# Kernel optimization log

Measured on AMD Instinct MI355X. Metric: run time of the kernel, lower is better.

Reference implementation:

```python
import jax, jax.numpy as jnp
import numpy as np

N, E, D, H, G = 100000, 1250000, 64, 64, 128
GRAPH_ATTR_DIM = 4
BN_EPS = 1e-5


def setup_inputs() -> dict:
    key = jax.random.key(0)
    ks = jax.random.split(key, 32)
    inp = {
        "x": jax.random.normal(ks[0], (N, D), dtype=jnp.float32),
        "edge_index": jax.random.randint(ks[1], (2, E), 0, N, dtype=jnp.int64),
        "batch": jnp.sort(jax.random.randint(ks[2], (N,), 0, G, dtype=jnp.int64)),
        "graph_attr": jax.random.normal(ks[3], (G, GRAPH_ATTR_DIM), dtype=jnp.float32),
    }
    # SAGEConv params per layer: lin_l (neighbor path, with bias), lin_r (self path, no bias)
    dims = [(D, H), (H, H), (H, H)]
    kidx = 4
    for i, (din, dout) in enumerate(dims):
        s = 1.0 / np.sqrt(din)
        inp[f"Wl{i}"] = jax.random.uniform(ks[kidx + 0], (din, dout), minval=-s, maxval=s, dtype=jnp.float32)
        inp[f"bl{i}"] = jax.random.uniform(ks[kidx + 1], (dout,), minval=-s, maxval=s, dtype=jnp.float32)
        inp[f"Wr{i}"] = jax.random.uniform(ks[kidx + 2], (din, dout), minval=-s, maxval=s, dtype=jnp.float32)
        # BatchNorm1d (eval mode: running stats)
        inp[f"g{i}"] = jnp.ones((dout,), jnp.float32)
        inp[f"be{i}"] = jnp.zeros((dout,), jnp.float32)
        inp[f"rm{i}"] = jax.random.normal(ks[kidx + 3], (dout,), dtype=jnp.float32) * 0.1
        inp[f"rv{i}"] = jax.random.uniform(ks[kidx + 4], (dout,), minval=0.5, maxval=1.5, dtype=jnp.float32)
        kidx += 5
    clf_in, clf_h = H + GRAPH_ATTR_DIM, H // 2
    s1 = 1.0 / np.sqrt(clf_in)
    s2 = 1.0 / np.sqrt(clf_h)
    inp["W1"] = jax.random.uniform(ks[kidx + 0], (clf_in, clf_h), minval=-s1, maxval=s1, dtype=jnp.float32)
    inp["b1"] = jax.random.uniform(ks[kidx + 1], (clf_h,), minval=-s1, maxval=s1, dtype=jnp.float32)
    inp["W2"] = jax.random.uniform(ks[kidx + 2], (clf_h, 2), minval=-s2, maxval=s2, dtype=jnp.float32)
    inp["b2"] = jax.random.uniform(ks[kidx + 3], (2,), minval=-s2, maxval=s2, dtype=jnp.float32)
    return inp


def _sage_conv(x, src, dst, Wl, bl, Wr):
    # mean-aggregate neighbor messages x[src] onto dst nodes
    msg = x[src]                                            # [E, d]
    agg = jax.ops.segment_sum(msg, dst, num_segments=N)     # [N, d]
    cnt = jax.ops.segment_sum(jnp.ones((src.shape[0],), x.dtype), dst, num_segments=N)
    agg = agg / jnp.maximum(cnt, 1.0)[:, None]
    return agg @ Wl + bl + x @ Wr


def _bn_eval(x, g, be, rm, rv):
    return (x - rm) * (g * jax.lax.rsqrt(rv + BN_EPS)) + be


def reference(x, edge_index, batch, graph_attr,
              Wl0, bl0, Wr0, g0, be0, rm0, rv0,
              Wl1, bl1, Wr1, g1, be1, rm1, rv1,
              Wl2, bl2, Wr2, g2, be2, rm2, rv2,
              W1, b1, W2, b2):
    src, dst = edge_index[0], edge_index[1]
    layer_params = [
        (Wl0, bl0, Wr0, g0, be0, rm0, rv0),
        (Wl1, bl1, Wr1, g1, be1, rm1, rv1),
        (Wl2, bl2, Wr2, g2, be2, rm2, rv2),
    ]
    h = x
    for (Wl, bl, Wr, g, be, rm, rv) in layer_params:
        h = jax.nn.relu(_bn_eval(_sage_conv(h, src, dst, Wl, bl, Wr), g, be, rm, rv))
        # dropout is identity in eval mode
    # global mean pool over graphs
    gsum = jax.ops.segment_sum(h, batch, num_segments=G)
    gcnt = jax.ops.segment_sum(jnp.ones((h.shape[0],), h.dtype), batch, num_segments=G)
    gemb = gsum / jnp.maximum(gcnt, 1.0)[:, None]
    gemb = jnp.concatenate([gemb, graph_attr], axis=1)      # [G, H+4]
    return jax.nn.relu(gemb @ W1 + b1) @ W2 + b2             # [G, 2]
```

## Files before the change

### kernel.cpp

```cpp
#include <hip/hip_runtime.h>
#include <hip/hip_fp16.h>

#define DIM 64
#define NGRAPH 128
#define GATTR 4
#define BN_EPS 1e-5f
#define SCAN_CHUNK 4096
#define NPASS 4
#define XS 17


__global__ __launch_bounds__(256) void k_zero(int* __restrict__ cnt, int n,
                                              float* __restrict__ gsum,
                                              int* __restrict__ gcnt) {
    int stride = gridDim.x * 256;
    for (int i = blockIdx.x * 256 + threadIdx.x; i < n; i += stride) cnt[i] = 0;
    int i0 = blockIdx.x * 256 + threadIdx.x;
    if (i0 < NGRAPH * DIM) gsum[i0] = 0.f;
    if (i0 < NGRAPH) gcnt[i0] = 0;
}


__global__ __launch_bounds__(256) void k_cast(const float4* __restrict__ x4,
                                              uint2* __restrict__ o, int n4) {
    int stride = gridDim.x * 256;
    for (int i = blockIdx.x * 256 + threadIdx.x; i < n4; i += stride) {
        float4 v = x4[i];
        __half2 a = __float22half2_rn(make_float2(v.x, v.y));
        __half2 b = __float22half2_rn(make_float2(v.z, v.w));
        uint2 u;
        u.x = *(unsigned int*)&a;
        u.y = *(unsigned int*)&b;
        o[i] = u;
    }
}


__global__ __launch_bounds__(256) void k_count(const int* __restrict__ dst,
                                               int* __restrict__ cnt, int E) {
    int e = blockIdx.x * blockDim.x + threadIdx.x;
    if (e < E) atomicAdd(&cnt[dst[e]], 1);
}

__global__ __launch_bounds__(256) void k_scan1(const int* __restrict__ cnt,
                                               int* __restrict__ rowptr,
                                               int* __restrict__ partials, int n) {
    __shared__ int ws[256];
    int tid = threadIdx.x;
    int base = blockIdx.x * SCAN_CHUNK + tid * 16;
    int v[16];
    int s = 0;
#pragma unroll
    for (int i = 0; i < 16; ++i) {
        int idx = base + i;
        v[i] = (idx < n) ? cnt[idx] : 0;
        s += v[i];
    }
    ws[tid] = s;
    __syncthreads();
    for (int off = 1; off < 256; off <<= 1) {
        int t = (tid >= off) ? ws[tid - off] : 0;
        __syncthreads();
        ws[tid] += t;
        __syncthreads();
    }
    int excl = (tid == 0) ? 0 : ws[tid - 1];
    if (tid == 255) partials[blockIdx.x] = ws[255];
#pragma unroll
    for (int i = 0; i < 16; ++i) {
        int idx = base + i;
        if (idx < n) rowptr[idx] = excl;
        excl += v[i];
    }
}

__global__ __launch_bounds__(256) void k_scan23(int* __restrict__ rowptr,
                                                int* __restrict__ wp,
                                                const int* __restrict__ partials,
                                                int n, int E) {
    __shared__ int soff;
    if (threadIdx.x == 0) {
        int s = 0;
        for (int j = 0; j < blockIdx.x; ++j) s += partials[j];
        soff = s;
    }
    __syncthreads();
    int off = soff;
    int base = blockIdx.x * SCAN_CHUNK;
    for (int i = threadIdx.x; i < SCAN_CHUNK; i += 256) {
        int idx = base + i;
        if (idx < n) {
            int v = rowptr[idx] + off;
            rowptr[idx] = v;
            wp[idx] = v;
        }
    }
    if (blockIdx.x == 0 && threadIdx.x == 0) rowptr[n] = E;
}

__global__ __launch_bounds__(256) void k_scatter_pass(const int* __restrict__ src,
                                                      const int* __restrict__ dst,
                                                      int* __restrict__ wp,
                                                      int* __restrict__ col,
                                                      int E, int lo, int hi) {
    int e = blockIdx.x * blockDim.x + threadIdx.x;
    if (e >= E) return;
    int d = dst[e];
    if (d < lo || d >= hi) return;
    int p = atomicAdd(&wp[d], 1);
    col[p] = src[e];
}


__global__ __launch_bounds__(256) void k_agg(const __half* __restrict__ h16,
                                             const int* __restrict__ row_ptr,
                                             const int* __restrict__ col,
                                             float* __restrict__ agg, int n) {
    int wid = (blockIdx.x * blockDim.x + threadIdx.x) >> 6;
    if (wid >= n) return;
    int lane = threadIdx.x & 63;
    int g = lane >> 3;
    int p = lane & 7;
    int beg = row_ptr[wid], end = row_ptr[wid + 1];

    float a0 = 0.f, a1 = 0.f, a2 = 0.f, a3 = 0.f;
    float a4 = 0.f, a5 = 0.f, a6 = 0.f, a7 = 0.f;

#define ACCUM(V)                                                          \
    {                                                                     \
        const __half2* q = (const __half2*)&(V);                          \
        float2 f0 = __half22float2(q[0]);                                 \
        float2 f1 = __half22float2(q[1]);                                 \
        float2 f2 = __half22float2(q[2]);                                 \
        float2 f3 = __half22float2(q[3]);                                 \
        a0 += f0.x; a1 += f0.y; a2 += f1.x; a3 += f1.y;                   \
        a4 += f2.x; a5 += f2.y; a6 += f3.x; a7 += f3.y;                   \
    }

    int j = beg + g;
    for (; j + 8 < end; j += 16) {
        int s0 = col[j];
        int s1 = col[j + 8];
        uint4 v0 = ((const uint4*)(h16 + (size_t)s0 * DIM))[p];
        uint4 v1 = ((const uint4*)(h16 + (size_t)s1 * DIM))[p];
        ACCUM(v0)
        ACCUM(v1)
    }
    if (j < end) {
        int s0 = col[j];
        uint4 v0 = ((const uint4*)(h16 + (size_t)s0 * DIM))[p];
        ACCUM(v0)
    }
#undef ACCUM

#pragma unroll
    for (int m = 8; m <= 32; m <<= 1) {
        a0 += __shfl_xor(a0, m, 64);
        a1 += __shfl_xor(a1, m, 64);
        a2 += __shfl_xor(a2, m, 64);
        a3 += __shfl_xor(a3, m, 64);
        a4 += __shfl_xor(a4, m, 64);
        a5 += __shfl_xor(a5, m, 64);
        a6 += __shfl_xor(a6, m, 64);
        a7 += __shfl_xor(a7, m, 64);
    }

    if (g == 0) {
        float c = (float)(end - beg);
        float inv = 1.0f / fmaxf(c, 1.0f);
        float4* op = (float4*)(agg + (size_t)wid * DIM + p * 8);
        float4 r0, r1;
        r0.x = a0 * inv; r0.y = a1 * inv; r0.z = a2 * inv; r0.w = a3 * inv;
        r1.x = a4 * inv; r1.y = a5 * inv; r1.z = a6 * inv; r1.w = a7 * inv;
        op[0] = r0;
        op[1] = r1;
    }
}


__global__ __launch_bounds__(256) void k_xform(const float* __restrict__ agg,
                                               const __half* __restrict__ h16,
                                               const float* __restrict__ Wl,
                                               const float* __restrict__ bl,
                                               const float* __restrict__ Wr,
                                               const float* __restrict__ bng,
                                               const float* __restrict__ bnb,
                                               const float* __restrict__ bnm,
                                               const float* __restrict__ bnv,
                                               __half* __restrict__ out16, int n) {
    __shared__ float4 sWl[64 * 16];
    __shared__ float4 sWr[64 * 16];
    __shared__ float4 sA[64 * XS];
    __shared__ float4 sH[64 * XS];
    int tid = threadIdx.x;
    int base = blockIdx.x * 64;
    int rows = min(64, n - base);

    const float4* Wl4 = (const float4*)Wl;
    const float4* Wr4 = (const float4*)Wr;
    const float4* A4 = (const float4*)(agg + (size_t)base * DIM);
    const uint2* H2 = (const uint2*)(h16 + (size_t)base * DIM);
    for (int i = tid; i < 1024; i += 256) {
        sWl[i] = Wl4[i];
        sWr[i] = Wr4[i];
        int row = i >> 4, c = i & 15;
        float4 va = {0.f, 0.f, 0.f, 0.f}, vh = {0.f, 0.f, 0.f, 0.f};
        if (row < rows) {
            va = A4[i];
            uint2 u = H2[i];
            const __half2* q = (const __half2*)&u;
            float2 lo = __half22float2(q[0]);
            float2 hi = __half22float2(q[1]);
            vh.x = lo.x; vh.y = lo.y; vh.z = hi.x; vh.w = hi.y;
        }
        sA[row * XS + c] = va;
        sH[row * XS + c] = vh;
    }
    __syncthreads();

    int dq = tid & 15;
    int nq = tid >> 4;
    float4 acc0 = {0.f, 0.f, 0.f, 0.f};
    float4 acc1 = {0.f, 0.f, 0.f, 0.f};
    float4 acc2 = {0.f, 0.f, 0.f, 0.f};
    float4 acc3 = {0.f, 0.f, 0.f, 0.f};

    int arow = nq * 4 * XS;
#pragma unroll 4
    for (int kg = 0; kg < 16; ++kg) {
        float4 wl0 = sWl[(kg * 4 + 0) * 16 + dq];
        float4 wl1 = sWl[(kg * 4 + 1) * 16 + dq];
        float4 wl2 = sWl[(kg * 4 + 2) * 16 + dq];
        float4 wl3 = sWl[(kg * 4 + 3) * 16 + dq];
        float4 wr0 = sWr[(kg * 4 + 0) * 16 + dq];
        float4 wr1 = sWr[(kg * 4 + 1) * 16 + dq];
        float4 wr2 = sWr[(kg * 4 + 2) * 16 + dq];
        float4 wr3 = sWr[(kg * 4 + 3) * 16 + dq];
        float4 a0 = sA[arow + 0 * XS + kg];
        float4 a1 = sA[arow + 1 * XS + kg];
        float4 a2 = sA[arow + 2 * XS + kg];
        float4 a3 = sA[arow + 3 * XS + kg];
        float4 h0 = sH[arow + 0 * XS + kg];
        float4 h1 = sH[arow + 1 * XS + kg];
        float4 h2 = sH[arow + 2 * XS + kg];
        float4 h3 = sH[arow + 3 * XS + kg];
#define ACC1(AC, AV, HV)                                                        \
        AC.x += AV.x * wl0.x + AV.y * wl1.x + AV.z * wl2.x + AV.w * wl3.x       \
              + HV.x * wr0.x + HV.y * wr1.x + HV.z * wr2.x + HV.w * wr3.x;      \
        AC.y += AV.x * wl0.y + AV.y * wl1.y + AV.z * wl2.y + AV.w * wl3.y       \
              + HV.x * wr0.y + HV.y * wr1.y + HV.z * wr2.y + HV.w * wr3.y;      \
        AC.z += AV.x * wl0.z + AV.y * wl1.z + AV.z * wl2.z + AV.w * wl3.z       \
              + HV.x * wr0.z + HV.y * wr1.z + HV.z * wr2.z + HV.w * wr3.z;      \
        AC.w += AV.x * wl0.w + AV.y * wl1.w + AV.z * wl2.w + AV.w * wl3.w       \
              + HV.x * wr0.w + HV.y * wr1.w + HV.z * wr2.w + HV.w * wr3.w;
        ACC1(acc0, a0, h0)
        ACC1(acc1, a1, h1)
        ACC1(acc2, a2, h2)
        ACC1(acc3, a3, h3)
#undef ACC1
    }

    float4 g4 = ((const float4*)bng)[dq];
    float4 v4 = ((const float4*)bnv)[dq];
    float4 be4 = ((const float4*)bnb)[dq];
    float4 rm4 = ((const float4*)bnm)[dq];
    float4 bi4 = ((const float4*)bl)[dq];
    float4 sc;
    sc.x = g4.x / sqrtf(v4.x + BN_EPS);
    sc.y = g4.y / sqrtf(v4.y + BN_EPS);
    sc.z = g4.z / sqrtf(v4.z + BN_EPS);
    sc.w = g4.w / sqrtf(v4.w + BN_EPS);

    float4* accp[4] = {&acc0, &acc1, &acc2, &acc3};
#pragma unroll
    for (int i = 0; i < 4; ++i) {
        int node = base + nq * 4 + i;
        if (node < n) {
            float4 a = *accp[i];
            float4 r;
            r.x = fmaxf((a.x + bi4.x - rm4.x) * sc.x + be4.x, 0.f);
            r.y = fmaxf((a.y + bi4.y - rm4.y) * sc.y + be4.y, 0.f);
            r.z = fmaxf((a.z + bi4.z - rm4.z) * sc.z + be4.z, 0.f);
            r.w = fmaxf((a.w + bi4.w - rm4.w) * sc.w + be4.w, 0.f);
            __half2 o01 = __float22half2_rn(make_float2(r.x, r.y));
            __half2 o23 = __float22half2_rn(make_float2(r.z, r.w));
            uint2 u;
            u.x = *(unsigned int*)&o01;
            u.y = *(unsigned int*)&o23;
            ((uint2*)(out16 + (size_t)node * DIM))[dq] = u;
        }
    }
}


__global__ __launch_bounds__(256) void k_pool(const __half* __restrict__ h16,
                                              const int* __restrict__ batch,
                                              float* __restrict__ gsum,
                                              int* __restrict__ gcnt, int n) {
    int nw = gridDim.x * 4;
    int w = blockIdx.x * 4 + (threadIdx.x >> 6);
    int lane = threadIdx.x & 63;
    int chunk = (n + nw - 1) / nw;
    int s = w * chunk, e = min(s + chunk, n);
    if (s >= e) return;
    int cur = batch[s];
    float acc = 0.f;
    int cnt = 0;
    for (int i = s; i < e; ++i) {
        int g = batch[i];
        if (g != cur) {
            atomicAdd(&gsum[cur * DIM + lane], acc);
            if (lane == 0) atomicAdd(&gcnt[cur], cnt);
            acc = 0.f; cnt = 0; cur = g;
        }
        acc += __half2float(h16[(size_t)i * DIM + lane]);
        ++cnt;
    }
    atomicAdd(&gsum[cur * DIM + lane], acc);
    if (lane == 0) atomicAdd(&gcnt[cur], cnt);
}


__global__ __launch_bounds__(256) void k_mlp(const float* __restrict__ gsum,
                                             const int* __restrict__ gcnt,
                                             const float* __restrict__ gattr,
                                             const float* __restrict__ W1,
                                             const float* __restrict__ b1,
                                             const float* __restrict__ W2,
                                             const float* __restrict__ b2,
                                             float* __restrict__ out) {
    __shared__ float emb[NGRAPH][DIM + GATTR];
    __shared__ float hid[NGRAPH][32];
    int tid = threadIdx.x;
    for (int i = tid; i < NGRAPH * DIM; i += 256) {
        int g = i >> 6, d = i & 63;
        float c = (float)gcnt[g];
        emb[g][d] = gsum[i] / fmaxf(c, 1.0f);
    }
    for (int i = tid; i < NGRAPH * GATTR; i += 256) {
        int g = i >> 2, d = i & 3;
        emb[g][DIM + d] = gattr[i];
    }
    __syncthreads();
    for (int t = tid; t < NGRAPH * 32; t += 256) {
        int g = t >> 5, j = t & 31;
        float a = b1[j];
        for (int k = 0; k < DIM + GATTR; ++k) a += emb[g][k] * W1[k * 32 + j];
        hid[g][j] = fmaxf(a, 0.f);
    }
    __syncthreads();
    {
        int g = tid >> 1, o = tid & 1;
        float a = b2[o];
        for (int k = 0; k < 32; ++k) a += hid[g][k] * W2[k * 2 + o];
        out[g * 2 + o] = a;
    }
}

extern "C" void kernel_launch(void* const* d_in, const int* in_sizes, int n_in,
                              void* d_out, int out_size, void* d_ws, size_t ws_size,
                              hipStream_t stream) {
    const float* x = (const float*)d_in[0];
    const int* ei = (const int*)d_in[1];
    const int* batch = (const int*)d_in[2];
    const float* gattr = (const float*)d_in[3];
    const int N = in_sizes[0] / DIM;
    const int E = in_sizes[1] / 2;
    const int* src = ei;
    const int* dst = ei + E;

    const float *Wl[3], *bl[3], *Wr[3], *bg[3], *bb[3], *bm[3], *bv[3];
    for (int l = 0; l < 3; ++l) {
        int base = 4 + l * 7;
        Wl[l] = (const float*)d_in[base + 0];
        bl[l] = (const float*)d_in[base + 1];
        Wr[l] = (const float*)d_in[base + 2];
        bg[l] = (const float*)d_in[base + 3];
        bb[l] = (const float*)d_in[base + 4];
        bm[l] = (const float*)d_in[base + 5];
        bv[l] = (const float*)d_in[base + 6];
    }
    const float* W1 = (const float*)d_in[25];
    const float* b1 = (const float*)d_in[26];
    const float* W2 = (const float*)d_in[27];
    const float* b2 = (const float*)d_in[28];

    char* ws = (char*)d_ws;
    size_t off = 0;
    auto alloc = [&](size_t bytes) -> char* {
        char* p = ws + off;
        off += (bytes + 255) & ~(size_t)255;
        return p;
    };
    int* cnt = (int*)alloc((size_t)N * 4);
    int* rowptr = (int*)alloc((size_t)(N + 1) * 4);
    int* wp = (int*)alloc((size_t)N * 4);
    int* col = (int*)alloc((size_t)E * 4);
    float* aggb = (float*)alloc((size_t)N * DIM * 4);
    __half* x16 = (__half*)alloc((size_t)N * DIM * 2);
    __half* h16a = (__half*)alloc((size_t)N * DIM * 2);
    __half* h16b = (__half*)alloc((size_t)N * DIM * 2);
    float* gsum = (float*)alloc((size_t)NGRAPH * DIM * 4);
    int* gcnt = (int*)alloc((size_t)NGRAPH * 4);
    int* partials = (int*)alloc(1024 * 4);
    (void)ws_size;

    const int tpb = 256;
    const int nscan = (N + SCAN_CHUNK - 1) / SCAN_CHUNK;
    const int nbE = (E + tpb - 1) / tpb;

    k_zero<<<512, tpb, 0, stream>>>(cnt, N, gsum, gcnt);
    k_cast<<<1024, tpb, 0, stream>>>((const float4*)x, (uint2*)x16, N * DIM / 4);
    k_count<<<nbE, tpb, 0, stream>>>(dst, cnt, E);
    k_scan1<<<nscan, tpb, 0, stream>>>(cnt, rowptr, partials, N);
    k_scan23<<<nscan, tpb, 0, stream>>>(rowptr, wp, partials, N, E);
    {
        int per = (N + NPASS - 1) / NPASS;
        for (int p = 0; p < NPASS; ++p) {
            int lo = p * per;
            int hi = min(lo + per, N);
            if (lo >= hi) break;
            k_scatter_pass<<<nbE, tpb, 0, stream>>>(src, dst, wp, col, E, lo, hi);
        }
    }

    const __half* hin = x16;
    __half* houts[3] = {h16a, h16b, h16a};
    for (int l = 0; l < 3; ++l) {
        k_agg<<<(N * 64 + tpb - 1) / tpb, tpb, 0, stream>>>(hin, rowptr, col, aggb, N);
        k_xform<<<(N + 63) / 64, 256, 0, stream>>>(aggb, hin, Wl[l], bl[l], Wr[l],
                                                   bg[l], bb[l], bm[l], bv[l], houts[l], N);
        hin = houts[l];
    }

    k_pool<<<256, tpb, 0, stream>>>(hin, batch, gsum, gcnt, N);
    k_mlp<<<1, tpb, 0, stream>>>(gsum, gcnt, gattr, W1, b1, W2, b2, (float*)d_out);
}
```

Baseline: 537.6 us.

## Replace atomic CSR build with two-level bucketed counting sort

Builds the CSR adjacency with a bucket-level radix sort instead of global per-node atomic counting plus four scatter passes. Each block histograms its edge chunk into 128-node buckets in shared memory, a global scan yields offsets, edges are binned as (src,dst) pairs staged through shared memory, and a per-bucket kernel does a local counting sort to emit rowptr and col. This removes heavy global atomics and repeated full passes over the edge list. The cost is extra kernels, a pairs buffer aliased onto the aggregation buffer, large shared-memory use in the binning kernel, and a serial prefix in the scan step over many partials.

```diff
diff --git a/kernel.cpp b/kernel.cpp
--- a/kernel.cpp
+++ b/kernel.cpp
@@ -6,15 +6,14 @@
 #define GATTR 4
 #define BN_EPS 1e-5f
 #define SCAN_CHUNK 4096
-#define NPASS 4
+#define SCHUNK 4096
+#define BUCKET_SHIFT 7
+#define BUCKET 128
 #define XS 17
 
 
-__global__ __launch_bounds__(256) void k_zero(int* __restrict__ cnt, int n,
-                                              float* __restrict__ gsum,
+__global__ __launch_bounds__(256) void k_zero(float* __restrict__ gsum,
                                               int* __restrict__ gcnt) {
-    int stride = gridDim.x * 256;
-    for (int i = blockIdx.x * 256 + threadIdx.x; i < n; i += stride) cnt[i] = 0;
     int i0 = blockIdx.x * 256 + threadIdx.x;
     if (i0 < NGRAPH * DIM) gsum[i0] = 0.f;
     if (i0 < NGRAPH) gcnt[i0] = 0;
@@ -36,15 +35,24 @@
 }
 
 
-__global__ __launch_bounds__(256) void k_count(const int* __restrict__ dst,
-                                               int* __restrict__ cnt, int E) {
-    int e = blockIdx.x * blockDim.x + threadIdx.x;
-    if (e < E) atomicAdd(&cnt[dst[e]], 1);
-}
-
-__global__ __launch_bounds__(256) void k_scan1(const int* __restrict__ cnt,
-                                               int* __restrict__ rowptr,
-                                               int* __restrict__ partials, int n) {
+__global__ __launch_bounds__(256) void k_bhist(const int* __restrict__ dst,
+                                               int* __restrict__ hist,
+                                               int E, int nb, int nbuck) {
+    __shared__ int lb[1024];
+    int tid = threadIdx.x, blk = blockIdx.x;
+    int base = blk * SCHUNK;
+    int cnt = min(SCHUNK, E - base);
+    for (int i = tid; i < nbuck; i += 256) lb[i] = 0;
+    __syncthreads();
+    for (int i = tid; i < cnt; i += 256)
+        atomicAdd(&lb[dst[base + i] >> BUCKET_SHIFT], 1);
+    __syncthreads();
+    for (int b = tid; b < nbuck; b += 256) hist[b * nb + blk] = lb[b];
+}
+
+__global__ __launch_bounds__(256) void k_gscan1(const int* __restrict__ in,
+                                                int* __restrict__ out,
+                                                int* __restrict__ partials, int n) {
     __shared__ int ws[256];
     int tid = threadIdx.x;
     int base = blockIdx.x * SCAN_CHUNK + tid * 16;
@@ -53,7 +61,7 @@
 #pragma unroll
     for (int i = 0; i < 16; ++i) {
         int idx = base + i;
-        v[i] = (idx < n) ? cnt[idx] : 0;
+        v[i] = (idx < n) ? in[idx] : 0;
         s += v[i];
     }
     ws[tid] = s;
@@ -69,15 +77,14 @@
 #pragma unroll
     for (int i = 0; i < 16; ++i) {
         int idx = base + i;
-        if (idx < n) rowptr[idx] = excl;
+        if (idx < n) out[idx] = excl;
         excl += v[i];
     }
 }
 
-__global__ __launch_bounds__(256) void k_scan23(int* __restrict__ rowptr,
-                                                int* __restrict__ wp,
-                                                const int* __restrict__ partials,
-                                                int n, int E) {
+__global__ __launch_bounds__(256) void k_gscan23(int* __restrict__ data,
+                                                 const int* __restrict__ partials,
+                                                 int n) {
     __shared__ int soff;
     if (threadIdx.x == 0) {
         int s = 0;
@@ -89,26 +96,122 @@
     int base = blockIdx.x * SCAN_CHUNK;
     for (int i = threadIdx.x; i < SCAN_CHUNK; i += 256) {
         int idx = base + i;
-        if (idx < n) {
-            int v = rowptr[idx] + off;
-            rowptr[idx] = v;
-            wp[idx] = v;
+        if (idx < n) data[idx] += off;
+    }
+}
+
+__global__ __launch_bounds__(256) void k_sbin(const int* __restrict__ src,
+                                              const int* __restrict__ dst,
+                                              const int* __restrict__ hist,
+                                              int2* __restrict__ pairs,
+                                              int E, int nb, int nbuck) {
+    __shared__ int lhist[1024];
+    __shared__ int lofs[1024];
+    __shared__ int lcur[1024];
+    __shared__ int lgb[1024];
+    __shared__ int ws[256];
+    __shared__ int2 stage[SCHUNK];
+    int tid = threadIdx.x, blk = blockIdx.x;
+    int base = blk * SCHUNK;
+    int cnt = min(SCHUNK, E - base);
+
+    for (int i = tid; i < nbuck; i += 256) lhist[i] = 0;
+    __syncthreads();
+
+    int2 mine[16];
+    int nmine = 0;
+    for (int i = tid; i < cnt; i += 256) {
+        int s = src[base + i];
+        int d = dst[base + i];
+        mine[nmine++] = make_int2(s, d);
+        atomicAdd(&lhist[d >> BUCKET_SHIFT], 1);
+    }
+    __syncthreads();
+
+    {
+        int b0 = tid * 4;
+        int v0 = (b0 + 0 < nbuck) ? lhist[b0 + 0] : 0;
+        int v1 = (b0 + 1 < nbuck) ? lhist[b0 + 1] : 0;
+        int v2 = (b0 + 2 < nbuck) ? lhist[b0 + 2] : 0;
+        int v3 = (b0 + 3 < nbuck) ? lhist[b0 + 3] : 0;
+        int s = v0 + v1 + v2 + v3;
+        ws[tid] = s;
+        __syncthreads();
+        for (int off = 1; off < 256; off <<= 1) {
+            int t = (tid >= off) ? ws[tid - off] : 0;
+            __syncthreads();
+            ws[tid] += t;
+            __syncthreads();
         }
-    }
-    if (blockIdx.x == 0 && threadIdx.x == 0) rowptr[n] = E;
-}
-
-__global__ __launch_bounds__(256) void k_scatter_pass(const int* __restrict__ src,
-                                                      const int* __restrict__ dst,
-                                                      int* __restrict__ wp,
-                                                      int* __restrict__ col,
-                                                      int E, int lo, int hi) {
-    int e = blockIdx.x * blockDim.x + threadIdx.x;
-    if (e >= E) return;
-    int d = dst[e];
-    if (d < lo || d >= hi) return;
-    int p = atomicAdd(&wp[d], 1);
-    col[p] = src[e];
+        int excl = (tid == 0) ? 0 : ws[tid - 1];
+        if (b0 + 0 < nbuck) lofs[b0 + 0] = excl;
+        excl += v0;
+        if (b0 + 1 < nbuck) lofs[b0 + 1] = excl;
+        excl += v1;
+        if (b0 + 2 < nbuck) lofs[b0 + 2] = excl;
+        excl += v2;
+        if (b0 + 3 < nbuck) lofs[b0 + 3] = excl;
+    }
+    __syncthreads();
+    for (int b = tid; b < nbuck; b += 256) {
+        lcur[b] = lofs[b];
+        lgb[b] = hist[b * nb + blk];
+    }
+    __syncthreads();
+
+    for (int j = 0; j < nmine; ++j) {
+        int b = mine[j].y >> BUCKET_SHIFT;
+        int pos = atomicAdd(&lcur[b], 1);
+        stage[pos] = mine[j];
+    }
+    __syncthreads();
+
+    for (int i = tid; i < cnt; i += 256) {
+        int2 pr = stage[i];
+        int b = pr.y >> BUCKET_SHIFT;
+        pairs[lgb[b] + (i - lofs[b])] = pr;
+    }
+}
+
+__global__ __launch_bounds__(256) void k_bsort(const int2* __restrict__ pairs,
+                                               const int* __restrict__ hist,
+                                               int* __restrict__ rowptr,
+                                               int* __restrict__ col,
+                                               int n, int nb, int nbuck, int E) {
+    __shared__ int lcnt[BUCKET];
+    __shared__ int lofs[BUCKET];
+    int b = blockIdx.x;
+    int tid = threadIdx.x;
+    int cbase = hist[b * nb];
+    int nxt = (b + 1 < nbuck) ? hist[(b + 1) * nb] : E;
+    int ecnt = nxt - cbase;
+    int node0 = b << BUCKET_SHIFT;
+    int nn = min(BUCKET, n - node0);
+    if (tid < BUCKET) lcnt[tid] = 0;
+    __syncthreads();
+    for (int i = tid; i < ecnt; i += 256)
+        atomicAdd(&lcnt[pairs[cbase + i].y - node0], 1);
+    __syncthreads();
+    int v = (tid < BUCKET) ? lcnt[tid] : 0;
+    if (tid < BUCKET) lofs[tid] = v;
+    __syncthreads();
+    for (int off = 1; off < BUCKET; off <<= 1) {
+        int t = (tid < BUCKET && tid >= off) ? lofs[tid - off] : 0;
+        __syncthreads();
+        if (tid < BUCKET) lofs[tid] += t;
+        __syncthreads();
+    }
+    int excl = (tid < BUCKET) ? (lofs[tid] - v) : 0;
+    __syncthreads();
+    if (tid < BUCKET) lofs[tid] = excl;
+    if (tid < nn) rowptr[node0 + tid] = cbase + excl;
+    __syncthreads();
+    for (int i = tid; i < ecnt; i += 256) {
+        int2 pr = pairs[cbase + i];
+        int p = cbase + atomicAdd(&lofs[pr.y - node0], 1);
+        col[p] = pr.x;
+    }
+    if (b == 0 && tid == 0) rowptr[n] = E;
 }
 
 
@@ -392,10 +495,13 @@
         off += (bytes + 255) & ~(size_t)255;
         return p;
     };
-    int* cnt = (int*)alloc((size_t)N * 4);
+    const int nb = (E + SCHUNK - 1) / SCHUNK;
+    const int nbuck = (N + BUCKET - 1) >> BUCKET_SHIFT;
+    const int total_h = nbuck * nb;
+
     int* rowptr = (int*)alloc((size_t)(N + 1) * 4);
-    int* wp = (int*)alloc((size_t)N * 4);
     int* col = (int*)alloc((size_t)E * 4);
+    int* hist = (int*)alloc((size_t)total_h * 4);
     float* aggb = (float*)alloc((size_t)N * DIM * 4);
     __half* x16 = (__half*)alloc((size_t)N * DIM * 2);
     __half* h16a = (__half*)alloc((size_t)N * DIM * 2);
@@ -403,26 +509,20 @@
     float* gsum = (float*)alloc((size_t)NGRAPH * DIM * 4);
     int* gcnt = (int*)alloc((size_t)NGRAPH * 4);
     int* partials = (int*)alloc(1024 * 4);
+    int2* pairs = (int2*)aggb;
     (void)ws_size;
 
     const int tpb = 256;
-    const int nscan = (N + SCAN_CHUNK - 1) / SCAN_CHUNK;
-    const int nbE = (E + tpb - 1) / tpb;
-
-    k_zero<<<512, tpb, 0, stream>>>(cnt, N, gsum, gcnt);
+    const int nscanH = (total_h + SCAN_CHUNK - 1) / SCAN_CHUNK;
+
+    k_zero<<<(NGRAPH * DIM + tpb - 1) / tpb, tpb, 0, stream>>>(gsum, gcnt);
     k_cast<<<1024, tpb, 0, stream>>>((const float4*)x, (uint2*)x16, N * DIM / 4);
-    k_count<<<nbE, tpb, 0, stream>>>(dst, cnt, E);
-    k_scan1<<<nscan, tpb, 0, stream>>>(cnt, rowptr, partials, N);
-    k_scan23<<<nscan, tpb, 0, stream>>>(rowptr, wp, partials, N, E);
-    {
-        int per = (N + NPASS - 1) / NPASS;
-        for (int p = 0; p < NPASS; ++p) {
-            int lo = p * per;
-            int hi = min(lo + per, N);
-            if (lo >= hi) break;
-            k_scatter_pass<<<nbE, tpb, 0, stream>>>(src, dst, wp, col, E, lo, hi);
-        }
-    }
+
+    k_bhist<<<nb, tpb, 0, stream>>>(dst, hist, E, nb, nbuck);
+    k_gscan1<<<nscanH, tpb, 0, stream>>>(hist, hist, partials, total_h);
+    k_gscan23<<<nscanH, tpb, 0, stream>>>(hist, partials, total_h);
+    k_sbin<<<nb, tpb, 0, stream>>>(src, dst, hist, pairs, E, nb, nbuck);
+    k_bsort<<<nbuck, tpb, 0, stream>>>(pairs, hist, rowptr, col, N, nb, nbuck, E);
 
     const __half* hin = x16;
     __half* houts[3] = {h16a, h16b, h16a};
```

Measured after the change: 454.7 us. 15.4% less time.
